# Kernel tuning notes

Hardware: AMD Instinct MI355X
Metric: run time of the kernel (lower is better)

## Reference

```python
import jax, jax.numpy as jnp
import numpy as np

B, T, E = 2, 2048, 1024
H = 16
HS = E // H  # 64
EPS = 1e-5


def _ln(x, g, b):
    mu = jnp.mean(x, axis=-1, keepdims=True)
    var = jnp.mean((x - mu) ** 2, axis=-1, keepdims=True)
    return (x - mu) * jax.lax.rsqrt(var + EPS) * g + b


def setup_inputs() -> dict:
    key = jax.random.key(0)
    ks = jax.random.split(key, 12)
    s_e = 1.0 / np.sqrt(E)
    s_h = 1.0 / np.sqrt(H * HS)
    s_f = 1.0 / np.sqrt(4 * E)
    return {
        "x": jax.random.normal(ks[0], (B, T, E), jnp.float32),
        # per-head Q/K/V weights stacked: [H, E, HS] (Linear bias=False)
        "Wq": jax.random.uniform(ks[1], (H, E, HS), jnp.float32, -s_e, s_e),
        "Wk": jax.random.uniform(ks[2], (H, E, HS), jnp.float32, -s_e, s_e),
        "Wv": jax.random.uniform(ks[3], (H, E, HS), jnp.float32, -s_e, s_e),
        # output projection: [H*HS, E]
        "Wp": jax.random.uniform(ks[4], (H * HS, E), jnp.float32, -s_h, s_h),
        "bp": jax.random.uniform(ks[5], (E,), jnp.float32, -s_h, s_h),
        # FFN
        "W1": jax.random.uniform(ks[6], (E, 4 * E), jnp.float32, -s_e, s_e),
        "b1": jax.random.uniform(ks[7], (4 * E,), jnp.float32, -s_e, s_e),
        "W2": jax.random.uniform(ks[8], (4 * E, E), jnp.float32, -s_f, s_f),
        "b2": jax.random.uniform(ks[9], (E,), jnp.float32, -s_f, s_f),
        # LayerNorms
        "g1": jnp.ones((E,), jnp.float32),
        "beta1": jnp.zeros((E,), jnp.float32),
        "g2": jnp.ones((E,), jnp.float32),
        "beta2": jnp.zeros((E,), jnp.float32),
    }


def reference(x, Wq, Wk, Wv, Wp, bp, W1, b1, W2, b2, g1, beta1, g2, beta2):
    # --- pre-LN + multi-head causal self-attention ---
    h = _ln(x, g1, beta1)                                   # [B,T,E]
    Q = jnp.einsum('bte,hed->bhtd', h, Wq)                  # [B,H,T,HS]
    K = jnp.einsum('bte,hed->bhtd', h, Wk)
    V = jnp.einsum('bte,hed->bhtd', h, Wv)
    scores = jnp.einsum('bhtd,bhsd->bhts', Q, K) * (HS ** -0.5)  # [B,H,T,T]
    mask = jnp.tril(jnp.ones((T, T), bool))
    scores = jnp.where(mask, scores, -jnp.inf)
    W = jax.nn.softmax(scores, axis=-1)                     # dropout p=0.0
    out = jnp.einsum('bhts,bhsd->bhtd', W, V)               # [B,H,T,HS]
    out = out.transpose(0, 2, 1, 3).reshape(B, T, H * HS)   # concat heads
    x = x + out @ Wp + bp                                   # residual 1
    # --- pre-LN + FFN ---
    h2 = _ln(x, g2, beta2)
    ff = jax.nn.relu(h2 @ W1 + b1) @ W2 + b2
    return x + ff
```

## Files before the change

kernel.cpp:

```cpp
#include <hip/hip_runtime.h>
#include <math.h>
#include <stdint.h>

typedef unsigned short u16;
typedef __attribute__((ext_vector_type(8))) short bf16x8;
typedef __attribute__((ext_vector_type(4))) float f32x4;

__device__ __forceinline__ u16 f2bf(float f) {
  unsigned int u = __float_as_uint(f);
  u += 0x7FFFu + ((u >> 16) & 1u);
  return (u16)(u >> 16);
}

__device__ __forceinline__ unsigned pkbf(float a, float b) {
  unsigned ua = __float_as_uint(a) + 0x8000u;
  unsigned ub = __float_as_uint(b) + 0x8000u;
  return __builtin_amdgcn_perm(ub, ua, 0x07060302u);
}

__device__ __forceinline__ void lds_barrier() {
  asm volatile("s_waitcnt lgkmcnt(0)\n\ts_barrier" ::: "memory");
}

__global__ __launch_bounds__(256) void transpose_bf16(
    const float* __restrict__ src, u16* __restrict__ dst,
    int R, int C, long sbs, long dbs, int drs, float scale) {
  __shared__ float tile[32][33];
  int c0 = blockIdx.x * 32, r0 = blockIdx.y * 32;
  long sb = (long)blockIdx.z * sbs, db = (long)blockIdx.z * dbs;
  int tx = threadIdx.x & 31, ty = threadIdx.x >> 5;
  #pragma unroll
  for (int k = 0; k < 4; ++k)
    tile[ty + k * 8][tx] = src[sb + (long)(r0 + ty + k * 8) * C + c0 + tx];
  __syncthreads();
  #pragma unroll
  for (int k = 0; k < 4; ++k)
    dst[db + (long)(c0 + ty + k * 8) * drs + r0 + tx] =
        f2bf(tile[tx][ty + k * 8] * scale);
}

__global__ __launch_bounds__(256) void vtrans(
    const u16* __restrict__ QKV, u16* __restrict__ VT) {
  __shared__ u16 Tl[64][72];
  int bt = blockIdx.x, h = blockIdx.y;
  int t = threadIdx.x;
  int r = t >> 3, c0 = (t & 7) << 3;
  const u16* src = QKV + (size_t)(bt * 64 + r) * 3072 + 2048 + h * 64 + c0;
  #pragma unroll
  for (int half = 0; half < 2; ++half) {
    bf16x8 v = *(const bf16x8*)(src + (size_t)(half * 32) * 3072);
    #pragma unroll
    for (int e = 0; e < 8; ++e) Tl[r + half * 32][c0 + e] = (u16)v[e];
  }
  __syncthreads();
  #pragma unroll
  for (int half = 0; half < 2; ++half) {
    int d = (t >> 3) + half * 32, s0 = (t & 7) << 3;
    bf16x8 o;
    #pragma unroll
    for (int e = 0; e < 8; ++e) o[e] = (short)Tl[s0 + e][d];
    *(bf16x8*)(VT + (size_t)(h * 64 + d) * 4096 + bt * 64 + s0) = o;
  }
}

__global__ __launch_bounds__(256) void ln_bf16(
    const float* __restrict__ x, const float* __restrict__ g,
    const float* __restrict__ b, u16* __restrict__ out) {
  int row = blockIdx.x;
  const float* xr = x + (size_t)row * 1024;
  int t = threadIdx.x;
  float4 v = *(const float4*)(xr + t * 4);
  float s = v.x + v.y + v.z + v.w;
  float q = v.x * v.x + v.y * v.y + v.z * v.z + v.w * v.w;
  #pragma unroll
  for (int off = 32; off >= 1; off >>= 1) {
    s += __shfl_xor(s, off);
    q += __shfl_xor(q, off);
  }
  __shared__ float ss[4], qq[4];
  int wid = t >> 6;
  if ((t & 63) == 0) { ss[wid] = s; qq[wid] = q; }
  __syncthreads();
  float st = ss[0] + ss[1] + ss[2] + ss[3];
  float qt = qq[0] + qq[1] + qq[2] + qq[3];
  float mean = st * (1.0f / 1024.0f);
  float var = qt * (1.0f / 1024.0f) - mean * mean;
  float rstd = rsqrtf(var + 1e-5f);
  float4 gv = *(const float4*)(g + t * 4);
  float4 bv = *(const float4*)(b + t * 4);
  uint2 st2;
  st2.x = pkbf((v.x - mean) * rstd * gv.x + bv.x, (v.y - mean) * rstd * gv.y + bv.y);
  st2.y = pkbf((v.z - mean) * rstd * gv.z + bv.z, (v.w - mean) * rstd * gv.w + bv.w);
  *(uint2*)(out + (size_t)row * 1024 + t * 4) = st2;
}

template <int BM, int BN>
__global__ __launch_bounds__(256) void gemm_bf16(
    const u16* __restrict__ A, const u16* __restrict__ Bt,
    const float* __restrict__ bias, const float* __restrict__ res,
    float* __restrict__ Cf, u16* __restrict__ Cb,
    int M, int N, int K, int relu) {
  constexpr int MI = BM / 32, NI = BN / 32;
  constexpr int ACH = BM / 32, BCH = BN / 32;
  __shared__ u16 As[2][BM * 64];
  __shared__ u16 Bs[2][BN * 64];
  int tid = threadIdx.x, wave = tid >> 6, lane = tid & 63;
  int wm = wave >> 1, wn = wave & 1;
  int lr = lane & 15, lq = lane >> 4;
  int lrow = lane >> 3, kblk = (lane & 7) ^ (lrow & 7);
  int g = blockIdx.x;
  int bm = ((((g & 7) << 2) | ((g >> 3) & 3))) * BM;
  int bn = (g >> 5) * BN;
  f32x4 acc[MI][NI];
  #pragma unroll
  for (int i = 0; i < MI; ++i)
    #pragma unroll
    for (int j = 0; j < NI; ++j) acc[i][j] = f32x4{0.f, 0.f, 0.f, 0.f};

  const u16* ag[ACH];
  #pragma unroll
  for (int j = 0; j < ACH; ++j) {
    int c = wave * ACH + j;
    ag[j] = A + (size_t)(bm + c * 8 + lrow) * K + kblk * 8;
  }
  const u16* bg[BCH];
  #pragma unroll
  for (int j = 0; j < BCH; ++j) {
    int c = wave * BCH + j;
    bg[j] = Bt + (size_t)(bn + c * 8 + lrow) * K + kblk * 8;
  }

  bf16x8 ra0[ACH], ra1[ACH], rb0[BCH], rb1[BCH];
  #pragma unroll
  for (int j = 0; j < ACH; ++j) { ra0[j] = *(const bf16x8*)(ag[j]); ra1[j] = *(const bf16x8*)(ag[j] + 64); }
  #pragma unroll
  for (int j = 0; j < BCH; ++j) { rb0[j] = *(const bf16x8*)(bg[j]); rb1[j] = *(const bf16x8*)(bg[j] + 64); }

  int nIter = K >> 6;

#define GEMM_STEP(BUF, RA, RB, IT)                                                         \
  {                                                                                        \
    _Pragma("unroll") for (int j = 0; j < ACH; ++j)                                        \
        *(bf16x8*)(&As[BUF][(wave * ACH + j) * 512 + lane * 8]) = RA[j];                   \
    _Pragma("unroll") for (int j = 0; j < BCH; ++j)                                        \
        *(bf16x8*)(&Bs[BUF][(wave * BCH + j) * 512 + lane * 8]) = RB[j];                   \
    lds_barrier();                                                                         \
    if ((IT) + 2 < nIter) {                                                                \
      int k0 = ((IT) + 2) << 6;                                                            \
      _Pragma("unroll") for (int j = 0; j < ACH; ++j) RA[j] = *(const bf16x8*)(ag[j] + k0); \
      _Pragma("unroll") for (int j = 0; j < BCH; ++j) RB[j] = *(const bf16x8*)(bg[j] + k0); \
    }                                                                                      \
    _Pragma("unroll") for (int kk = 0; kk < 2; ++kk) {                                     \
      bf16x8 af[MI], bfr[NI];                                                              \
      _Pragma("unroll") for (int mi = 0; mi < MI; ++mi)                                    \
          af[mi] = *(const bf16x8*)(&As[BUF][(wm * (BM / 2) + mi * 16 + lr) * 64 +         \
                                             (((kk << 2) + lq) ^ (lr & 7)) * 8]);          \
      _Pragma("unroll") for (int ni = 0; ni < NI; ++ni)                                    \
          bfr[ni] = *(const bf16x8*)(&Bs[BUF][(wn * (BN / 2) + ni * 16 + lr) * 64 +        \
                                              (((kk << 2) + lq) ^ (lr & 7)) * 8]);         \
      _Pragma("unroll") for (int mi = 0; mi < MI; ++mi)                                    \
          _Pragma("unroll") for (int ni = 0; ni < NI; ++ni)                                \
              acc[mi][ni] = __builtin_amdgcn_mfma_f32_16x16x32_bf16(bfr[ni], af[mi],       \
                                                                    acc[mi][ni], 0, 0, 0); \
    }                                                                                      \
    lds_barrier();                                                                         \
  }

  for (int it = 0; it < nIter; it += 2) {
    GEMM_STEP(0, ra0, rb0, it)
    GEMM_STEP(1, ra1, rb1, it + 1)
  }
#undef GEMM_STEP

  #pragma unroll
  for (int mi = 0; mi < MI; ++mi) {
    int row = bm + wm * (BM / 2) + mi * 16 + lr;
    #pragma unroll
    for (int ni = 0; ni < NI; ++ni) {
      int col = bn + wn * (BN / 2) + ni * 16 + lq * 4;
      f32x4 v = acc[mi][ni];
      if (bias) {
        float4 bb = *(const float4*)(bias + col);
        v[0] += bb.x; v[1] += bb.y; v[2] += bb.z; v[3] += bb.w;
      }
      if (res) {
        float4 rv = *(const float4*)(res + (size_t)row * N + col);
        v[0] += rv.x; v[1] += rv.y; v[2] += rv.z; v[3] += rv.w;
      }
      if (relu) {
        #pragma unroll
        for (int e = 0; e < 4; ++e) v[e] = fmaxf(v[e], 0.f);
      }
      if (Cb) {
        uint2 w;
        w.x = pkbf(v[0], v[1]);
        w.y = pkbf(v[2], v[3]);
        *(uint2*)(Cb + (size_t)row * N + col) = w;
      } else {
        float4 o;
        o.x = v[0]; o.y = v[1]; o.z = v[2]; o.w = v[3];
        *(float4*)(Cf + (size_t)row * N + col) = o;
      }
    }
  }
}

__global__ __launch_bounds__(256) void attn_mfma(
    const u16* __restrict__ QKV, const u16* __restrict__ VT,
    u16* __restrict__ O) {
  __shared__ u16 Klds[2][64 * 64];
  __shared__ u16 Vl[2][64 * 64];
  __shared__ u16 Pl[4][16 * 72];
  int i = blockIdx.x;
  int qtA = i, qtB = 31 - i;
  int b = blockIdx.y >> 4, hh = blockIdx.y & 15;
  int tid = threadIdx.x, wave = tid >> 6, lane = tid & 63;
  int lr = lane & 15, lq = lane >> 4;
  int lrow = lane >> 3, kb = (lane & 7) ^ (lrow & 7);

  const u16* qbase = QKV + (size_t)(b * 2048) * 3072 + hh * 64 + lq * 8;
  int qrA = qtA * 64 + wave * 16 + lr, qrB = qtB * 64 + wave * 16 + lr;
  bf16x8 qA0 = *(const bf16x8*)(qbase + (size_t)qrA * 3072);
  bf16x8 qA1 = *(const bf16x8*)(qbase + (size_t)qrA * 3072 + 32);
  bf16x8 qB0 = *(const bf16x8*)(qbase + (size_t)qrB * 3072);
  bf16x8 qB1 = *(const bf16x8*)(qbase + (size_t)qrB * 3072 + 32);

  f32x4 ofA[4], ofB[4];
  float lA = 0.f, lB = 0.f;
  #pragma unroll
  for (int d = 0; d < 4; ++d) {
    ofA[d] = f32x4{0.f, 0.f, 0.f, 0.f};
    ofB[d] = f32x4{0.f, 0.f, 0.f, 0.f};
  }

  const u16* kg[2];
  const u16* vg[2];
  #pragma unroll
  for (int j = 0; j < 2; ++j) {
    int c = wave * 2 + j;
    kg[j] = QKV + (size_t)(b * 2048 + c * 8 + lrow) * 3072 + 1024 + hh * 64 + kb * 8;
    vg[j] = VT + (size_t)(hh * 64 + c * 8 + lrow) * 4096 + b * 2048 + kb * 8;
  }
  bf16x8 rk[2], rv[2];
  #pragma unroll
  for (int j = 0; j < 2; ++j) {
    rk[j] = *(const bf16x8*)(kg[j]);
    rv[j] = *(const bf16x8*)(vg[j]);
  }

#define ATTN_TILE(Q0, Q1, QT, OF, LSUM)                                                    \
  {                                                                                        \
    f32x4 sf[4];                                                                           \
    _Pragma("unroll") for (int ni = 0; ni < 4; ++ni) sf[ni] = f32x4{0.f, 0.f, 0.f, 0.f};   \
    _Pragma("unroll") for (int ni = 0; ni < 4; ++ni) {                                     \
      int rowk = ni * 16 + lr;                                                             \
      bf16x8 k0 = *(const bf16x8*)(&Klds[buf][rowk * 64 + ((lq) ^ (lr & 7)) * 8]);         \
      bf16x8 k1 = *(const bf16x8*)(&Klds[buf][rowk * 64 + ((4 + lq) ^ (lr & 7)) * 8]);     \
      sf[ni] = __builtin_amdgcn_mfma_f32_16x16x32_bf16(k0, Q0, sf[ni], 0, 0, 0);           \
      sf[ni] = __builtin_amdgcn_mfma_f32_16x16x32_bf16(k1, Q1, sf[ni], 0, 0, 0);           \
    }                                                                                      \
    if (kt == (QT)) {                                                                      \
      _Pragma("unroll") for (int ni = 0; ni < 4; ++ni)                                     \
          _Pragma("unroll") for (int r = 0; r < 4; ++r)                                    \
              if (ni * 16 + lq * 4 + r > wave * 16 + lr) sf[ni][r] = -1e30f;               \
    }                                                                                      \
    _Pragma("unroll") for (int ni = 0; ni < 4; ++ni) {                                     \
      float p0 = exp2f(sf[ni][0]), p1 = exp2f(sf[ni][1]);                                  \
      float p2 = exp2f(sf[ni][2]), p3 = exp2f(sf[ni][3]);                                  \
      LSUM += (p0 + p1) + (p2 + p3);                                                       \
      uint2 w;                                                                             \
      w.x = pkbf(p0, p1);                                                                  \
      w.y = pkbf(p2, p3);                                                                  \
      *(uint2*)(&Pl[wave][lr * 72 + ni * 16 + lq * 4]) = w;                                \
    }                                                                                      \
    bf16x8 pf0 = *(const bf16x8*)(&Pl[wave][lr * 72 + lq * 8]);                            \
    bf16x8 pf1 = *(const bf16x8*)(&Pl[wave][lr * 72 + 32 + lq * 8]);                       \
    _Pragma("unroll") for (int di = 0; di < 4; ++di) {                                     \
      int rowv = di * 16 + lr;                                                             \
      bf16x8 v0 = *(const bf16x8*)(&Vl[buf][rowv * 64 + ((lq) ^ (lr & 7)) * 8]);           \
      bf16x8 v1 = *(const bf16x8*)(&Vl[buf][rowv * 64 + ((4 + lq) ^ (lr & 7)) * 8]);       \
      OF[di] = __builtin_amdgcn_mfma_f32_16x16x32_bf16(v0, pf0, OF[di], 0, 0, 0);          \
      OF[di] = __builtin_amdgcn_mfma_f32_16x16x32_bf16(v1, pf1, OF[di], 0, 0, 0);          \
    }                                                                                      \
  }

  for (int kt = 0; kt <= qtB; ++kt) {
    int buf = kt & 1;
    #pragma unroll
    for (int j = 0; j < 2; ++j) {
      *(bf16x8*)(&Klds[buf][(wave * 2 + j) * 512 + lane * 8]) = rk[j];
      *(bf16x8*)(&Vl[buf][(wave * 2 + j) * 512 + lane * 8]) = rv[j];
    }
    lds_barrier();
    if (kt < qtB) {
      #pragma unroll
      for (int j = 0; j < 2; ++j) {
        rk[j] = *(const bf16x8*)(kg[j] + (size_t)(kt + 1) * 64 * 3072);
        rv[j] = *(const bf16x8*)(vg[j] + (kt + 1) * 64);
      }
    }
    ATTN_TILE(qB0, qB1, qtB, ofB, lB)
    if (kt <= qtA) ATTN_TILE(qA0, qA1, qtA, ofA, lA)
    lds_barrier();
  }
#undef ATTN_TILE

  lB += __shfl_xor(lB, 16);
  lB += __shfl_xor(lB, 32);
  lA += __shfl_xor(lA, 16);
  lA += __shfl_xor(lA, 32);
  float invB = 1.0f / lB, invA = 1.0f / lA;
  u16* opB = O + (size_t)(b * 2048 + qtB * 64 + wave * 16 + lr) * 1024 + hh * 64;
  u16* opA = O + (size_t)(b * 2048 + qtA * 64 + wave * 16 + lr) * 1024 + hh * 64;
  #pragma unroll
  for (int di = 0; di < 4; ++di) {
    uint2 wB, wA;
    wB.x = pkbf(ofB[di][0] * invB, ofB[di][1] * invB);
    wB.y = pkbf(ofB[di][2] * invB, ofB[di][3] * invB);
    wA.x = pkbf(ofA[di][0] * invA, ofA[di][1] * invA);
    wA.y = pkbf(ofA[di][2] * invA, ofA[di][3] * invA);
    *(uint2*)(opB + di * 16 + lq * 4) = wB;
    *(uint2*)(opA + di * 16 + lq * 4) = wA;
  }
}

extern "C" void kernel_launch(void* const* d_in, const int* in_sizes, int n_in,
                              void* d_out, int out_size, void* d_ws, size_t ws_size,
                              hipStream_t stream) {
  const float* x   = (const float*)d_in[0];
  const float* Wq  = (const float*)d_in[1];
  const float* Wk  = (const float*)d_in[2];
  const float* Wv  = (const float*)d_in[3];
  const float* Wp  = (const float*)d_in[4];
  const float* bp  = (const float*)d_in[5];
  const float* W1  = (const float*)d_in[6];
  const float* b1  = (const float*)d_in[7];
  const float* W2  = (const float*)d_in[8];
  const float* b2  = (const float*)d_in[9];
  const float* g1  = (const float*)d_in[10];
  const float* be1 = (const float*)d_in[11];
  const float* g2  = (const float*)d_in[12];
  const float* be2 = (const float*)d_in[13];
  float* out = (float*)d_out;

  u16* ws16   = (u16*)d_ws;
  u16* Wqkv_t = ws16;
  u16* Wp_t   = Wqkv_t + 3145728;
  u16* W1_t   = Wp_t + 1048576;
  u16* W2_t   = W1_t + 4194304;
  u16* h      = W2_t + 4194304;
  u16* QKV    = h + 4194304;
  u16* Obuf   = QKV + 12582912;
  u16* f      = QKV;
  float* x1   = (float*)(Obuf + 4194304);
  u16* VT     = (u16*)(x1 + 4194304);

  const float qsc = 0.18033688f;
  transpose_bf16<<<dim3(2, 32, 16), 256, 0, stream>>>(Wq, Wqkv_t, 1024, 64, 65536, 65536, 1024, qsc);
  transpose_bf16<<<dim3(2, 32, 16), 256, 0, stream>>>(Wk, Wqkv_t + 1048576, 1024, 64, 65536, 65536, 1024, 1.f);
  transpose_bf16<<<dim3(2, 32, 16), 256, 0, stream>>>(Wv, Wqkv_t + 2097152, 1024, 64, 65536, 65536, 1024, 1.f);
  transpose_bf16<<<dim3(32, 32, 1), 256, 0, stream>>>(Wp, Wp_t, 1024, 1024, 0, 0, 1024, 1.f);
  transpose_bf16<<<dim3(128, 32, 1), 256, 0, stream>>>(W1, W1_t, 1024, 4096, 0, 0, 1024, 1.f);
  transpose_bf16<<<dim3(32, 128, 1), 256, 0, stream>>>(W2, W2_t, 4096, 1024, 0, 0, 4096, 1.f);

  ln_bf16<<<4096, 256, 0, stream>>>(x, g1, be1, h);
  gemm_bf16<128, 128><<<768, 256, 0, stream>>>(h, Wqkv_t, nullptr, nullptr,
                                               nullptr, QKV, 4096, 3072, 1024, 0);
  vtrans<<<dim3(64, 16), 256, 0, stream>>>(QKV, VT);
  attn_mfma<<<dim3(16, 32), 256, 0, stream>>>(QKV, VT, Obuf);
  gemm_bf16<128, 64><<<512, 256, 0, stream>>>(Obuf, Wp_t, bp, x,
                                              x1, nullptr, 4096, 1024, 1024, 0);
  ln_bf16<<<4096, 256, 0, stream>>>(x1, g2, be2, h);
  gemm_bf16<128, 128><<<1024, 256, 0, stream>>>(h, W1_t, b1, nullptr,
                                                nullptr, f, 4096, 4096, 1024, 1);
  gemm_bf16<128, 64><<<512, 256, 0, stream>>>(f, W2_t, b2, x1,
                                              out, nullptr, 4096, 1024, 4096, 0);
}
```

Baseline: 347.5 us.

## Add 256x128-tile GEMM for QKV/FFN1, enlarge tiles, drop redundant LDS barriers

Adds a new gemm_big kernel with a 256x128 block tile and 4x8 MFMA accumulators per wave. It is used for the QKV projection and the first FFN layer, with the aim of raising data reuse per LDS load and cutting global traffic. The Wp and W2 GEMMs move from 128x64 to 128x128 tiles. The trailing barrier in the double-buffered GEMM and attention loops is removed, since the ping-pong buffers already keep reads and writes apart. The trade-offs are fewer blocks (about one wave of blocks on 256 CUs) and heavy register pressure in the new kernel, which could reduce latency hiding.

```diff
diff --git a/kernel.cpp b/kernel.cpp
--- a/kernel.cpp
+++ b/kernel.cpp
@@ -92,6 +92,109 @@
   st2.x = pkbf((v.x - mean) * rstd * gv.x + bv.x, (v.y - mean) * rstd * gv.y + bv.y);
   st2.y = pkbf((v.z - mean) * rstd * gv.z + bv.z, (v.w - mean) * rstd * gv.w + bv.w);
   *(uint2*)(out + (size_t)row * 1024 + t * 4) = st2;
+}
+
+__global__ __launch_bounds__(256, 1) void gemm_big(
+    const u16* __restrict__ A, const u16* __restrict__ Bt,
+    const float* __restrict__ bias, float* __restrict__ Cf,
+    u16* __restrict__ Cb, int N, int K, int relu) {
+  __shared__ u16 As[2][256 * 64];
+  __shared__ u16 Bs[2][128 * 64];
+  int tid = threadIdx.x, wave = tid >> 6, lane = tid & 63;
+  int lr = lane & 15, lq = lane >> 4;
+  int lrow = lane >> 3, kblk = (lane & 7) ^ (lrow & 7);
+  int g = blockIdx.x;
+  int bm = ((((g & 7) << 1) | ((g >> 3) & 1))) * 256;
+  int bn = (g >> 4) * 128;
+  f32x4 acc[4][8];
+  #pragma unroll
+  for (int i = 0; i < 4; ++i)
+    #pragma unroll
+    for (int j = 0; j < 8; ++j) acc[i][j] = f32x4{0.f, 0.f, 0.f, 0.f};
+
+  const u16* ag[8];
+  #pragma unroll
+  for (int j = 0; j < 8; ++j) {
+    int c = wave * 8 + j;
+    ag[j] = A + (size_t)(bm + c * 8 + lrow) * K + kblk * 8;
+  }
+  const u16* bg[4];
+  #pragma unroll
+  for (int j = 0; j < 4; ++j) {
+    int c = wave * 4 + j;
+    bg[j] = Bt + (size_t)(bn + c * 8 + lrow) * K + kblk * 8;
+  }
+
+  bf16x8 ra[8], rb[4];
+  #pragma unroll
+  for (int j = 0; j < 8; ++j) ra[j] = *(const bf16x8*)(ag[j]);
+  #pragma unroll
+  for (int j = 0; j < 4; ++j) rb[j] = *(const bf16x8*)(bg[j]);
+
+  int nIter = K >> 6;
+  for (int it = 0; it < nIter; ++it) {
+    int buf = it & 1;
+    #pragma unroll
+    for (int j = 0; j < 8; ++j)
+      *(bf16x8*)(&As[buf][(wave * 8 + j) * 512 + lane * 8]) = ra[j];
+    #pragma unroll
+    for (int j = 0; j < 4; ++j)
+      *(bf16x8*)(&Bs[buf][(wave * 4 + j) * 512 + lane * 8]) = rb[j];
+    lds_barrier();
+    if (it + 1 < nIter) {
+      int k0 = (it + 1) << 6;
+      #pragma unroll
+      for (int j = 0; j < 8; ++j) ra[j] = *(const bf16x8*)(ag[j] + k0);
+      #pragma unroll
+      for (int j = 0; j < 4; ++j) rb[j] = *(const bf16x8*)(bg[j] + k0);
+    }
+    #pragma unroll
+    for (int kk = 0; kk < 2; ++kk) {
+      bf16x8 af[4], bf[8];
+      #pragma unroll
+      for (int mi = 0; mi < 4; ++mi)
+        af[mi] = *(const bf16x8*)(&As[buf][(wave * 64 + mi * 16 + lr) * 64 +
+                                           (((kk << 2) + lq) ^ (lr & 7)) * 8]);
+      #pragma unroll
+      for (int ni = 0; ni < 8; ++ni)
+        bf[ni] = *(const bf16x8*)(&Bs[buf][(ni * 16 + lr) * 64 +
+                                           (((kk << 2) + lq) ^ (lr & 7)) * 8]);
+      #pragma unroll
+      for (int mi = 0; mi < 4; ++mi)
+        #pragma unroll
+        for (int ni = 0; ni < 8; ++ni)
+          acc[mi][ni] = __builtin_amdgcn_mfma_f32_16x16x32_bf16(bf[ni], af[mi],
+                                                                acc[mi][ni], 0, 0, 0);
+    }
+  }
+
+  #pragma unroll
+  for (int mi = 0; mi < 4; ++mi) {
+    int row = bm + wave * 64 + mi * 16 + lr;
+    #pragma unroll
+    for (int ni = 0; ni < 8; ++ni) {
+      int col = bn + ni * 16 + lq * 4;
+      f32x4 v = acc[mi][ni];
+      if (bias) {
+        float4 bb = *(const float4*)(bias + col);
+        v[0] += bb.x; v[1] += bb.y; v[2] += bb.z; v[3] += bb.w;
+      }
+      if (relu) {
+        #pragma unroll
+        for (int e = 0; e < 4; ++e) v[e] = fmaxf(v[e], 0.f);
+      }
+      if (Cb) {
+        uint2 w;
+        w.x = pkbf(v[0], v[1]);
+        w.y = pkbf(v[2], v[3]);
+        *(uint2*)(Cb + (size_t)row * N + col) = w;
+      } else {
+        float4 o;
+        o.x = v[0]; o.y = v[1]; o.z = v[2]; o.w = v[3];
+        *(float4*)(Cf + (size_t)row * N + col) = o;
+      }
+    }
+  }
 }
 
 template <int BM, int BN>
@@ -163,7 +266,6 @@
               acc[mi][ni] = __builtin_amdgcn_mfma_f32_16x16x32_bf16(bfr[ni], af[mi],       \
                                                                     acc[mi][ni], 0, 0, 0); \
     }                                                                                      \
-    lds_barrier();                                                                         \
   }
 
   for (int it = 0; it < nIter; it += 2) {
@@ -301,7 +403,6 @@
     }
     ATTN_TILE(qB0, qB1, qtB, ofB, lB)
     if (kt <= qtA) ATTN_TILE(qA0, qA1, qtA, ofA, lA)
-    lds_barrier();
   }
 #undef ATTN_TILE
 
@@ -364,15 +465,13 @@
   transpose_bf16<<<dim3(32, 128, 1), 256, 0, stream>>>(W2, W2_t, 4096, 1024, 0, 0, 4096, 1.f);
 
   ln_bf16<<<4096, 256, 0, stream>>>(x, g1, be1, h);
-  gemm_bf16<128, 128><<<768, 256, 0, stream>>>(h, Wqkv_t, nullptr, nullptr,
-                                               nullptr, QKV, 4096, 3072, 1024, 0);
+  gemm_big<<<384, 256, 0, stream>>>(h, Wqkv_t, nullptr, nullptr, QKV, 3072, 1024, 0);
   vtrans<<<dim3(64, 16), 256, 0, stream>>>(QKV, VT);
   attn_mfma<<<dim3(16, 32), 256, 0, stream>>>(QKV, VT, Obuf);
-  gemm_bf16<128, 64><<<512, 256, 0, stream>>>(Obuf, Wp_t, bp, x,
-                                              x1, nullptr, 4096, 1024, 1024, 0);
+  gemm_bf16<128, 128><<<256, 256, 0, stream>>>(Obuf, Wp_t, bp, x,
+                                               x1, nullptr, 4096, 1024, 1024, 0);
   ln_bf16<<<4096, 256, 0, stream>>>(x1, g2, be2, h);
-  gemm_bf16<128, 128><<<1024, 256, 0, stream>>>(h, W1_t, b1, nullptr,
-                                                nullptr, f, 4096, 4096, 1024, 1);
-  gemm_bf16<128, 64><<<512, 256, 0, stream>>>(f, W2_t, b2, x1,
-                                              out, nullptr, 4096, 1024, 4096, 0);
-}
+  gemm_big<<<512, 256, 0, stream>>>(h, W1_t, b1, nullptr, f, 4096, 1024, 1);
+  gemm_bf16<128, 128><<<256, 256, 0, stream>>>(f, W2_t, b2, x1,
+                                               out, nullptr, 4096, 1024, 4096, 0);
+}
```

Measured after the change: 384.1 us. 1.11x slower.
